# Kernel optimization log

Measured on AMD Instinct MI355X. Metric: run time of the kernel, lower is better.

Reference implementation:

```python
import jax, jax.numpy as jnp
import numpy as np

INPUT_CHANNELS = 6
RESERVOIR_SIZE = 256
SPECTRAL_RADIUS = 0.9
SPARSITY = 0.8
BATCH = 256
SEQ_LEN = 512


def _make_reservoir_weights(seed=0):
    rng = np.random.RandomState(seed)
    W_res = rng.randn(RESERVOIR_SIZE, RESERVOIR_SIZE).astype(np.float32)
    mask = (rng.rand(RESERVOIR_SIZE, RESERVOIR_SIZE) > SPARSITY).astype(np.float32)
    W_res = W_res * mask
    cur_radius = np.abs(np.linalg.eigvals(W_res)).max()
    if cur_radius > 0:
        W_res = W_res * (SPECTRAL_RADIUS / cur_radius)
    return W_res.astype(np.float32)


def setup_inputs() -> dict:
    key = jax.random.key(0)
    k_x, k_in = jax.random.split(key)
    x = jax.random.normal(k_x, (BATCH, SEQ_LEN, INPUT_CHANNELS), dtype=jnp.float32)
    W_in = jax.random.normal(k_in, (INPUT_CHANNELS, RESERVOIR_SIZE), dtype=jnp.float32) * 0.1
    W_res = jnp.asarray(_make_reservoir_weights())
    return {"x": x, "W_in": W_in, "W_res": W_res}


def reference(x, W_in, W_res):
    # x: [B, T, C] -> x_proj: [B, T, R]
    x_proj = jnp.einsum("btc,cr->btr", x, W_in)
    B = x.shape[0]
    R = W_res.shape[0]
    h0 = jnp.zeros((B, R), dtype=x.dtype)

    def step(h, xp_t):
        # xp_t: [B, R]
        h_new = jnp.tanh(xp_t + h @ W_res)
        return h_new, h_new

    # scan over time: xs must be time-major [T, B, R]
    _, h_seq = jax.lax.scan(step, h0, jnp.swapaxes(x_proj, 0, 1))
    return jnp.swapaxes(h_seq, 0, 1)  # [B, T, R]
```

## Files before the change

### kernel.cpp

```cpp
#include <hip/hip_runtime.h>

#define BATCH 256
#define SEQ_T 512
#define CIN   6
#define RES   256
#define HPAD  272

template <int CTRL>
__device__ __forceinline__ float quad_xor_add(float v) {
    union { float f; int i; } u;
    u.f = v;
    u.i = __builtin_amdgcn_mov_dpp(u.i, CTRL, 0xF, 0xF, true);
    return v + u.f;
}

__global__ __launch_bounds__(1024, 1)
void esn_scan_kernel(const float* __restrict__ x,
                     const float* __restrict__ W_in,
                     const float* __restrict__ W_res,
                     float* __restrict__ out) {
    __shared__ float h[2][HPAD];

    const int tid  = threadIdx.x;
    const int b    = blockIdx.x;
    const int lane = tid & 63;
    const int wid  = tid >> 6;
    const int sub  = lane & 3;
    const int rr   = lane >> 2;
    const int r    = (wid << 4) | rr;

    float w[64];
    #pragma unroll
    for (int j = 0; j < 64; ++j)
        w[j] = W_res[(sub * 64 + j) * RES + r];

    float win[CIN];
    #pragma unroll
    for (int c = 0; c < CIN; ++c) win[c] = W_in[c * RES + r];

    if (tid < RES) h[0][tid + ((tid >> 6) << 2)] = 0.0f;
    __syncthreads();

    const float* xb = x + (size_t)b * SEQ_T * CIN;
    float*       ob = out + (size_t)b * SEQ_T * RES + r;

    const int wr = r + ((r >> 6) << 2);
    const float4* hA = (const float4*)&h[0][sub * 68];
    const float4* hB = (const float4*)&h[1][sub * 68];
    float* hAw = &h[0][wr];
    float* hBw = &h[1][wr];

#define ESN_STEP(HRD, HWR)                                              \
    {                                                                   \
        float xv[CIN];                                                  \
        _Pragma("unroll")                                               \
        for (int c = 0; c < CIN; ++c) xv[c] = xb[c];                    \
        xb += CIN;                                                      \
        float a0 = 0.f, a1 = 0.f, a2 = 0.f, a3 = 0.f;                   \
        _Pragma("unroll")                                               \
        for (int j = 0; j < 16; ++j) {                                  \
            float4 hv = (HRD)[j];                                       \
            a0 = fmaf(hv.x, w[4*j+0], a0);                              \
            a1 = fmaf(hv.y, w[4*j+1], a1);                              \
            a2 = fmaf(hv.z, w[4*j+2], a2);                              \
            a3 = fmaf(hv.w, w[4*j+3], a3);                              \
        }                                                               \
        float s = (a0 + a1) + (a2 + a3);                                \
        s = quad_xor_add<0xB1>(s);                        \
        s = quad_xor_add<0x4E>(s);                        \
        if (sub == 0) {                                                 \
            _Pragma("unroll")                                           \
            for (int c = 0; c < CIN; ++c) s = fmaf(xv[c], win[c], s);   \
            float e  = __expf(2.0f * s);                                \
            float hn = 1.0f - 2.0f * __builtin_amdgcn_rcpf(e + 1.0f);   \
            *(HWR) = hn;                                                \
            *ob = hn;                                                   \
        }                                                               \
        ob += RES;                                                      \
        asm volatile("s_waitcnt lgkmcnt(0)" ::: "memory");              \
        __builtin_amdgcn_s_barrier();                                   \
        asm volatile("" ::: "memory");                                  \
    }

    for (int t = 0; t < SEQ_T; t += 2) {
        ESN_STEP(hA, hBw);
        ESN_STEP(hB, hAw);
    }
#undef ESN_STEP
}

extern "C" void kernel_launch(void* const* d_in, const int* in_sizes, int n_in,
                              void* d_out, int out_size, void* d_ws, size_t ws_size,
                              hipStream_t stream) {
    const float* x     = (const float*)d_in[0];
    const float* W_in  = (const float*)d_in[1];
    const float* W_res = (const float*)d_in[2];
    float*       out   = (float*)d_out;

    esn_scan_kernel<<<BATCH, 1024, 0, stream>>>(x, W_in, W_res, out);
}
```

Before: 523.4 us.

## Split reduction 16-way per output quad with row-rotate DPP reductions

Each thread now computes partial dot products for 4 reservoir outputs over a 16-element chunk of h, instead of 1 output over 64 elements. Per step, each thread reads only 4 float4 values from LDS instead of 16, and each loaded h value feeds four outputs. The cross-lane reduction becomes a 16-lane row-rotate DPP tree across four accumulators, with four writer lanes per group. The aim is to cut LDS read traffic on the serial per-step critical path, at the cost of more DPP ops and an extra select chain.

```diff
diff --git a/kernel.cpp b/kernel.cpp
--- a/kernel.cpp
+++ b/kernel.cpp
@@ -4,10 +4,12 @@
 #define SEQ_T 512
 #define CIN   6
 #define RES   256
-#define HPAD  272
+#define NCHUNK  16
+#define CSTRIDE 20
+#define HBUF    (NCHUNK * CSTRIDE)
 
 template <int CTRL>
-__device__ __forceinline__ float quad_xor_add(float v) {
+__device__ __forceinline__ float dpp_ror_add(float v) {
     union { float f; int i; } u;
     u.f = v;
     u.i = __builtin_amdgcn_mov_dpp(u.i, CTRL, 0xF, 0xF, true);
@@ -19,56 +21,84 @@
                      const float* __restrict__ W_in,
                      const float* __restrict__ W_res,
                      float* __restrict__ out) {
-    __shared__ float h[2][HPAD];
+    __shared__ float h[2][HBUF];
 
     const int tid  = threadIdx.x;
     const int b    = blockIdx.x;
     const int lane = tid & 63;
     const int wid  = tid >> 6;
-    const int sub  = lane & 3;
-    const int rr   = lane >> 2;
-    const int r    = (wid << 4) | rr;
+    const int sub  = lane & 15;
+    const int rg   = lane >> 4;
 
-    float w[64];
+    const int rbase = (wid << 4) | (rg << 2);
+
+    float w[4][16];
     #pragma unroll
-    for (int j = 0; j < 64; ++j)
-        w[j] = W_res[(sub * 64 + j) * RES + r];
+    for (int a = 0; a < 4; ++a)
+        #pragma unroll
+        for (int j = 0; j < 16; ++j)
+            w[a][j] = W_res[(sub * 16 + j) * RES + rbase + a];
 
+    const int ract = rbase + (sub & 3);
     float win[CIN];
     #pragma unroll
-    for (int c = 0; c < CIN; ++c) win[c] = W_in[c * RES + r];
+    for (int c = 0; c < CIN; ++c) win[c] = W_in[c * RES + ract];
 
-    if (tid < RES) h[0][tid + ((tid >> 6) << 2)] = 0.0f;
+    if (tid < HBUF) h[0][tid] = 0.0f;
     __syncthreads();
 
     const float* xb = x + (size_t)b * SEQ_T * CIN;
-    float*       ob = out + (size_t)b * SEQ_T * RES + r;
+    float*       ob = out + (size_t)b * SEQ_T * RES + ract;
 
-    const int wr = r + ((r >> 6) << 2);
-    const float4* hA = (const float4*)&h[0][sub * 68];
-    const float4* hB = (const float4*)&h[1][sub * 68];
-    float* hAw = &h[0][wr];
-    float* hBw = &h[1][wr];
+    const float4* hr0 = (const float4*)&h[0][sub * CSTRIDE];
+    const float4* hr1 = (const float4*)&h[1][sub * CSTRIDE];
+    const int wslot = wid * CSTRIDE + (rg << 2) + (sub & 3);
+    float* hw0 = &h[0][wslot];
+    float* hw1 = &h[1][wslot];
+    const bool writer = (sub < 4);
 
 #define ESN_STEP(HRD, HWR)                                              \
     {                                                                   \
+        float4 h0 = (HRD)[0], h1 = (HRD)[1], h2 = (HRD)[2], h3 = (HRD)[3]; \
         float xv[CIN];                                                  \
         _Pragma("unroll")                                               \
-        for (int c = 0; c < CIN; ++c) xv[c] = xb[c];                    \
+        for (int c = 0; c < CIN; ++c) xv[c] = xb[c];    \
         xb += CIN;                                                      \
-        float a0 = 0.f, a1 = 0.f, a2 = 0.f, a3 = 0.f;                   \
+        float acc[4];                                                   \
         _Pragma("unroll")                                               \
-        for (int j = 0; j < 16; ++j) {                                  \
-            float4 hv = (HRD)[j];                                       \
-            a0 = fmaf(hv.x, w[4*j+0], a0);                              \
-            a1 = fmaf(hv.y, w[4*j+1], a1);                              \
-            a2 = fmaf(hv.z, w[4*j+2], a2);                              \
-            a3 = fmaf(hv.w, w[4*j+3], a3);                              \
+        for (int a = 0; a < 4; ++a) {                                   \
+            float s0 = h0.x * w[a][0];                                  \
+            s0 = fmaf(h0.y, w[a][1], s0);                               \
+            s0 = fmaf(h0.z, w[a][2], s0);                               \
+            s0 = fmaf(h0.w, w[a][3], s0);                               \
+            float s1 = h1.x * w[a][4];                                  \
+            s1 = fmaf(h1.y, w[a][5], s1);                               \
+            s1 = fmaf(h1.z, w[a][6], s1);                               \
+            s1 = fmaf(h1.w, w[a][7], s1);                               \
+            float s2 = h2.x * w[a][8];                                  \
+            s2 = fmaf(h2.y, w[a][9],  s2);                              \
+            s2 = fmaf(h2.z, w[a][10], s2);                              \
+            s2 = fmaf(h2.w, w[a][11], s2);                              \
+            float s3 = h3.x * w[a][12];                                 \
+            s3 = fmaf(h3.y, w[a][13], s3);                              \
+            s3 = fmaf(h3.z, w[a][14], s3);                              \
+            s3 = fmaf(h3.w, w[a][15], s3);                              \
+            acc[a] = (s0 + s1) + (s2 + s3);                             \
         }                                                               \
-        float s = (a0 + a1) + (a2 + a3);                                \
-        s = quad_xor_add<0xB1>(s);                        \
-        s = quad_xor_add<0x4E>(s);                        \
-        if (sub == 0) {                                                 \
+         \
+        _Pragma("unroll")                                               \
+        for (int a = 0; a < 4; ++a) acc[a] = dpp_ror_add<0x128>(acc[a]); \
+        _Pragma("unroll")                                               \
+        for (int a = 0; a < 4; ++a) acc[a] = dpp_ror_add<0x124>(acc[a]); \
+        _Pragma("unroll")                                               \
+        for (int a = 0; a < 4; ++a) acc[a] = dpp_ror_add<0x122>(acc[a]); \
+        _Pragma("unroll")                                               \
+        for (int a = 0; a < 4; ++a) acc[a] = dpp_ror_add<0x121>(acc[a]); \
+        float s = acc[0];                                               \
+        s = (sub == 1) ? acc[1] : s;                                    \
+        s = (sub == 2) ? acc[2] : s;                                    \
+        s = (sub == 3) ? acc[3] : s;                                    \
+        if (writer) {                                                   \
             _Pragma("unroll")                                           \
             for (int c = 0; c < CIN; ++c) s = fmaf(xv[c], win[c], s);   \
             float e  = __expf(2.0f * s);                                \
@@ -83,8 +113,8 @@
     }
 
     for (int t = 0; t < SEQ_T; t += 2) {
-        ESN_STEP(hA, hBw);
-        ESN_STEP(hB, hAw);
+        ESN_STEP(hr0, hw1);
+        ESN_STEP(hr1, hw0);
     }
 #undef ESN_STEP
 }
```

Result: faster. 473.7 us (-9.5%).

## Split each dot product over 8 lanes and use packed FMA

Applied to the files above, without the earlier changes.

The recurrent matvec is re-tiled. Each 8-lane group now computes two output rows, with each lane covering a 32-element chunk of h. This halves the LDS float4 reads per thread per step, and v_pk_fma_f32 halves the FMA instruction count. The reduction becomes a three-stage DPP chain, and the next step's x inputs are prefetched ahead of the barrier. The cost is an extra DPP stage, a select between the two row sums, and a new padded LDS layout for h.

```diff
diff --git a/kernel.cpp b/kernel.cpp
--- a/kernel.cpp
+++ b/kernel.cpp
@@ -4,10 +4,20 @@
 #define SEQ_T 512
 #define CIN   6
 #define RES   256
-#define HPAD  272
+#define NCH     8
+#define CSTRIDE 36
+#define HBUF    (NCH * CSTRIDE)
+
+typedef float f32x2 __attribute__((ext_vector_type(2)));
+
+__device__ __forceinline__ f32x2 pk_fma(f32x2 a, f32x2 b, f32x2 c) {
+    f32x2 d;
+    asm("v_pk_fma_f32 %0, %1, %2, %3" : "=v"(d) : "v"(a), "v"(b), "v"(c));
+    return d;
+}
 
 template <int CTRL>
-__device__ __forceinline__ float quad_xor_add(float v) {
+__device__ __forceinline__ float dpp_add(float v) {
     union { float f; int i; } u;
     u.f = v;
     u.i = __builtin_amdgcn_mov_dpp(u.i, CTRL, 0xF, 0xF, true);
@@ -19,58 +29,81 @@
                      const float* __restrict__ W_in,
                      const float* __restrict__ W_res,
                      float* __restrict__ out) {
-    __shared__ float h[2][HPAD];
+    __shared__ float h[2][HBUF];
 
     const int tid  = threadIdx.x;
     const int b    = blockIdx.x;
     const int lane = tid & 63;
     const int wid  = tid >> 6;
-    const int sub  = lane & 3;
-    const int rr   = lane >> 2;
-    const int r    = (wid << 4) | rr;
+    const int sub  = lane & 7;
+    const int rg   = lane >> 3;
 
-    float w[64];
+    const int rbase = (wid << 4) | (rg << 1);
+
+    f32x2 w2[2][16];
     #pragma unroll
-    for (int j = 0; j < 64; ++j)
-        w[j] = W_res[(sub * 64 + j) * RES + r];
+    for (int a = 0; a < 2; ++a)
+        #pragma unroll
+        for (int j = 0; j < 16; ++j) {
+            f32x2 p;
+            p.x = W_res[(sub * 32 + 2 * j)     * RES + rbase + a];
+            p.y = W_res[(sub * 32 + 2 * j + 1) * RES + rbase + a];
+            w2[a][j] = p;
+        }
 
+    const int ract = rbase + (sub & 1);
     float win[CIN];
     #pragma unroll
-    for (int c = 0; c < CIN; ++c) win[c] = W_in[c * RES + r];
+    for (int c = 0; c < CIN; ++c) win[c] = W_in[c * RES + ract];
 
-    if (tid < RES) h[0][tid + ((tid >> 6) << 2)] = 0.0f;
+    if (tid < HBUF) h[0][tid] = 0.0f;
     __syncthreads();
 
     const float* xb = x + (size_t)b * SEQ_T * CIN;
-    float*       ob = out + (size_t)b * SEQ_T * RES + r;
+    float*       ob = out + (size_t)b * SEQ_T * RES + ract;
 
-    const int wr = r + ((r >> 6) << 2);
-    const float4* hA = (const float4*)&h[0][sub * 68];
-    const float4* hB = (const float4*)&h[1][sub * 68];
-    float* hAw = &h[0][wr];
-    float* hBw = &h[1][wr];
+    const float4* hr0 = (const float4*)&h[0][sub * CSTRIDE];
+    const float4* hr1 = (const float4*)&h[1][sub * CSTRIDE];
+    const int wslot = ((ract >> 5) * CSTRIDE) + (ract & 31);
+    float* hw0 = &h[0][wslot];
+    float* hw1 = &h[1][wslot];
+    const bool writer = (sub < 2);
 
-#define ESN_STEP(HRD, HWR)                                              \
+    float xA[CIN], xB[CIN];
+    #pragma unroll
+    for (int c = 0; c < CIN; ++c) xA[c] = xb[c];
+    xb += CIN;
+
+#define ESN_STEP(HRD, HWR, XC, XN, PREF)                                \
     {                                                                   \
-        float xv[CIN];                                                  \
+        float4 hv[NCH];                                                 \
         _Pragma("unroll")                                               \
-        for (int c = 0; c < CIN; ++c) xv[c] = xb[c];                    \
-        xb += CIN;                                                      \
-        float a0 = 0.f, a1 = 0.f, a2 = 0.f, a3 = 0.f;                   \
+        for (int j = 0; j < NCH; ++j) hv[j] = (HRD)[j];                 \
+        if (PREF) {                                                     \
+            _Pragma("unroll")                                           \
+            for (int c = 0; c < CIN; ++c) (XN)[c] = xb[c];              \
+            xb += CIN;                                                  \
+        }                                                               \
+        f32x2 acc0 = {0.f, 0.f}, acc1 = {0.f, 0.f};                    \
         _Pragma("unroll")                                               \
-        for (int j = 0; j < 16; ++j) {                                  \
-            float4 hv = (HRD)[j];                                       \
-            a0 = fmaf(hv.x, w[4*j+0], a0);                              \
-            a1 = fmaf(hv.y, w[4*j+1], a1);                              \
-            a2 = fmaf(hv.z, w[4*j+2], a2);                              \
-            a3 = fmaf(hv.w, w[4*j+3], a3);                              \
+        for (int j = 0; j < NCH; ++j) {                                 \
+            f32x2 plo, phi;                                             \
+            plo.x = hv[j].x; plo.y = hv[j].y;                           \
+            phi.x = hv[j].z; phi.y = hv[j].w;                           \
+            acc0 = pk_fma(plo, w2[0][2 * j],     acc0);                 \
+            acc0 = pk_fma(phi, w2[0][2 * j + 1], acc0);                 \
+            acc1 = pk_fma(plo, w2[1][2 * j],     acc1);                 \
+            acc1 = pk_fma(phi, w2[1][2 * j + 1], acc1);                 \
         }                                                               \
-        float s = (a0 + a1) + (a2 + a3);                                \
-        s = quad_xor_add<0xB1>(s);                        \
-        s = quad_xor_add<0x4E>(s);                        \
-        if (sub == 0) {                                                 \
+        float a0 = acc0.x + acc0.y;                                     \
+        float a1 = acc1.x + acc1.y;                                     \
+        a0 = dpp_add<0xB1>(a0);  a1 = dpp_add<0xB1>(a1);                \
+        a0 = dpp_add<0x4E>(a0);  a1 = dpp_add<0x4E>(a1);                \
+        a0 = dpp_add<0x141>(a0); a1 = dpp_add<0x141>(a1);               \
+        float s = (sub & 1) ? a1 : a0;                                  \
+        if (writer) {                                                   \
             _Pragma("unroll")                                           \
-            for (int c = 0; c < CIN; ++c) s = fmaf(xv[c], win[c], s);   \
+            for (int c = 0; c < CIN; ++c) s = fmaf((XC)[c], win[c], s); \
             float e  = __expf(2.0f * s);                                \
             float hn = 1.0f - 2.0f * __builtin_amdgcn_rcpf(e + 1.0f);   \
             *(HWR) = hn;                                                \
@@ -82,10 +115,12 @@
         asm volatile("" ::: "memory");                                  \
     }
 
-    for (int t = 0; t < SEQ_T; t += 2) {
-        ESN_STEP(hA, hBw);
-        ESN_STEP(hB, hAw);
+    for (int t = 0; t < SEQ_T - 2; t += 2) {
+        ESN_STEP(hr0, hw1, xA, xB, 1);
+        ESN_STEP(hr1, hw0, xB, xA, 1);
     }
+    ESN_STEP(hr0, hw1, xA, xB, 1);
+    ESN_STEP(hr1, hw0, xB, xA, 0);
 #undef ESN_STEP
 }
 
```

Measured after the change: 466.2 us. 1.12x faster.
